# Optimization experiments

Measured on AMD Instinct MI355X. Metric: run time of the kernel, lower is better.

## Reference

```python
import jax, jax.numpy as jnp
import numpy as np
from jax import lax

H = 8  # hardcoded in the module (node indices 0..7)


def setup_inputs() -> dict:
    k = jax.random.key(0)
    k1, k2, k3, k4, k5 = jax.random.split(k, 5)
    B, S, D = 1024, 7, 4096  # seq MUST be 7 (Conv1d uses it as channels)
    query = jax.random.normal(k1, (B, S, D), jnp.float32)
    key = jax.random.normal(k2, (B, S, D), jnp.float32)
    value = jax.random.normal(k3, (B, S, D), jnp.float32)
    conv_w = jax.random.normal(k4, (7, 7, 3), jnp.float32) * 0.05  # Conv1d(7,7,3) OIW
    conv_b = jnp.zeros((7,), jnp.float32)
    w_out = jax.random.normal(k5, (D, D), jnp.float32) * 0.02  # linears[-1].weight
    b_out = jnp.zeros((D,), jnp.float32)
    return {"query": query, "key": key, "value": value,
            "conv_w": conv_w, "conv_b": conv_b, "w_out": w_out, "b_out": b_out}


def reference(query, key, value, conv_w, conv_b, w_out, b_out):
    B, S, D = query.shape
    dk = D // H
    # split q/k/v into H chunks of d_k along last dim -> [B, H, S, dk]
    split = lambda t: jnp.moveaxis(t.reshape(B, S, H, dk), 2, 1)
    q, kk, v = split(query), split(key), split(value)
    # node_i = cat(key_i, value_i, query_i) -> [B, H, S, 3dk]
    node = jnp.concatenate([kk, v, q], axis=-1)
    # neighbor sums along the head axis: s0=n0+n1, s_i=n_{i-1}+n_i+n_{i+1}, s7=n6+n7
    npad = jnp.pad(node, ((0, 0), (1, 1), (0, 0), (0, 0)))
    s = npad[:, :-2] + npad[:, 1:-1] + npad[:, 2:]  # [B, H, S, 3dk]
    # shared Conv1d(7,7,3,stride=1,pad=1) over the 3dk axis; channels = S = 7
    x = s.reshape(B * H, S, 3 * dk)
    x = lax.conv_general_dilated(x, conv_w, window_strides=(1,), padding=((1, 1),),
                                 dimension_numbers=("NCW", "OIW", "NCW"))
    x = x + conv_b[None, :, None]
    x = x.reshape(B, H, S, 3 * dk)
    # re-split: [0]=k', [1]=v', [2]=q'; attention(q', k', v')
    k2, v2, q2 = x[..., :dk], x[..., dk:2 * dk], x[..., 2 * dk:]
    scores = jnp.einsum("bhqd,bhkd->bhqk", q2, k2) * (1.0 / (dk ** 0.5))
    p = jax.nn.softmax(scores, axis=-1)
    atn = jnp.einsum("bhqk,bhkd->bhqd", p, v2)  # [B, H, S, dk]
    out = jnp.moveaxis(atn, 1, 2).reshape(B, S, D)  # concat heads
    return out @ w_out.T + b_out  # linears[-1]
```

## Files before the change

kernel.cpp:

```cpp
#include <hip/hip_runtime.h>
#include <hip/hip_bf16.h>

#define Hh 8
#define Bb 1024
#define Ss 7
#define Dd 4096
#define DK 512
#define Mrows (Bb*Ss)
#define RS 520

typedef float  f32x4  __attribute__((ext_vector_type(4)));
typedef float  f32x2  __attribute__((ext_vector_type(2)));
typedef short  bf16x8 __attribute__((ext_vector_type(8)));

static __device__ __forceinline__ unsigned short f2bf(float f) {
  union { float f; unsigned int u; } v; v.f = f;
  unsigned int u = v.u;
  u += 0x7FFFu + ((u >> 16) & 1u);
  return (unsigned short)(u >> 16);
}

static __device__ __forceinline__ void gload_lds16(const void* g, void* l) {
  __builtin_amdgcn_global_load_lds(
      (const __attribute__((address_space(1))) unsigned int*)g,
      (__attribute__((address_space(3))) unsigned int*)l,
      16, 0, 0);
}

static __device__ __forceinline__ float sum3s(const float* __restrict__ src, int b, int i, int h, int c) {
  long base = (long)(b * Ss + i) * Dd + h * DK + c;
  float v = src[base];
  if (h > 0) v += src[base - DK];
  if (h < 7) v += src[base + DK];
  return v;
}

__global__ __launch_bounds__(256, 5) void attn_kernel(
    const float* __restrict__ qg, const float* __restrict__ kg, const float* __restrict__ vg,
    const float* __restrict__ cw, const float* __restrict__ cb,
    unsigned short* __restrict__ Abf)
{
  __shared__ float bufA[Ss][RS];
  __shared__ float bufB[Ss][RS];
  __shared__ float cw4[49][4];
  __shared__ float cb_s[7];
  __shared__ float scores_s[49];
  __shared__ float pmat[7][7];

  const int t    = threadIdx.x;
  const int bh   = blockIdx.x;
  const int b    = bh >> 3, h = bh & 7;
  const int lane = t & 63, wave = t >> 6;

  if (t < 147) { int oi = t / 3; cw4[oi][t - oi * 3] = cw[t]; }
  if (t < 7) {
    cb_s[t] = cb[t];
    bufA[t][3]   = 0.f;
    bufA[t][516] = sum3s(vg, b, t, h, 0);
    bufB[t][3]   = sum3s(vg, b, t, h, 511);
    bufB[t][516] = 0.f;
  }

  #pragma unroll
  for (int j = 0; j < 7; ++j) {
    int slot = j * 256 + t;
    int isK  = slot < 896;
    int s2   = isK ? slot : slot - 896;
    int i    = s2 >> 7, c4 = (s2 & 127) << 2;
    const float* src = isK ? kg : qg;
    float* dst = isK ? &bufA[i][4 + c4] : &bufB[i][4 + c4];
    long base = (long)(b * Ss + i) * Dd + h * DK + c4;
    float4 v = *(const float4*)(src + base);
    if (h > 0) { float4 a = *(const float4*)(src + base - DK); v.x+=a.x; v.y+=a.y; v.z+=a.z; v.w+=a.w; }
    if (h < 7) { float4 a = *(const float4*)(src + base + DK); v.x+=a.x; v.y+=a.y; v.z+=a.z; v.w+=a.w; }
    *(float4*)dst = v;
  }
  __syncthreads();

  const int w2 = 2 * t;
  float ok0[7], ok1[7], oq0[7], oq1[7];
  #pragma unroll
  for (int o = 0; o < 7; ++o) { float c0 = cb_s[o]; ok0[o]=c0; ok1[o]=c0; oq0[o]=c0; oq1[o]=c0; }
  #pragma unroll
  for (int i = 0; i < 7; ++i) {
    float a0 = bufA[i][3+w2], a1 = bufA[i][4+w2], a2 = bufA[i][5+w2], a3 = bufA[i][6+w2];
    float q0 = bufB[i][3+w2], q1 = bufB[i][4+w2], q2 = bufB[i][5+w2], q3 = bufB[i][6+w2];
    #pragma unroll
    for (int o = 0; o < 7; ++o) {
      f32x4 wv = *(const f32x4*)&cw4[o*7+i][0];
      ok0[o] += wv[0]*a0 + wv[1]*a1 + wv[2]*a2;
      ok1[o] += wv[0]*a1 + wv[1]*a2 + wv[2]*a3;
      oq0[o] += wv[0]*q0 + wv[1]*q1 + wv[2]*q2;
      oq1[o] += wv[0]*q1 + wv[1]*q2 + wv[2]*q3;
    }
  }
  __syncthreads();
  #pragma unroll
  for (int o = 0; o < 7; ++o) {
    *(f32x2*)&bufA[o][4 + w2] = (f32x2){ok0[o], ok1[o]};
    *(f32x2*)&bufB[o][4 + w2] = (f32x2){oq0[o], oq1[o]};
  }
  __syncthreads();

  for (int p = wave; p < 49; p += 4) {
    int qq = p / 7, kk = p - qq * 7;
    f32x4 x0 = *(const f32x4*)&bufB[qq][4 + lane * 4];
    f32x4 x1 = *(const f32x4*)&bufB[qq][4 + 256 + lane * 4];
    f32x4 y0 = *(const f32x4*)&bufA[kk][4 + lane * 4];
    f32x4 y1 = *(const f32x4*)&bufA[kk][4 + 256 + lane * 4];
    float part = x0[0]*y0[0] + x0[1]*y0[1] + x0[2]*y0[2] + x0[3]*y0[3]
               + x1[0]*y1[0] + x1[1]*y1[1] + x1[2]*y1[2] + x1[3]*y1[3];
    #pragma unroll
    for (int off = 32; off; off >>= 1) part += __shfl_xor(part, off);
    if (lane == 0) scores_s[p] = part * 0.044194173824159216f;
  }
  __syncthreads();

  if (t < 7) {
    float row[7], m = -1e30f;
    #pragma unroll
    for (int k = 0; k < 7; ++k) { row[k] = scores_s[t * 7 + k]; m = fmaxf(m, row[k]); }
    float s = 0.f;
    #pragma unroll
    for (int k = 0; k < 7; ++k) { row[k] = __expf(row[k] - m); s += row[k]; }
    float inv = 1.0f / s;
    #pragma unroll
    for (int k = 0; k < 7; ++k) pmat[t][k] = row[k] * inv;
    bufB[t][3]   = sum3s(kg, b, t, h, 511);
    bufB[t][516] = sum3s(qg, b, t, h, 0);
  }
  #pragma unroll
  for (int j = 0; j < 4; ++j) {
    int slot = j * 256 + t;
    if (slot < 896) {
      int i = slot >> 7, c4 = (slot & 127) << 2;
      long base = (long)(b * Ss + i) * Dd + h * DK + c4;
      float4 v = *(const float4*)(vg + base);
      if (h > 0) { float4 a = *(const float4*)(vg + base - DK); v.x+=a.x; v.y+=a.y; v.z+=a.z; v.w+=a.w; }
      if (h < 7) { float4 a = *(const float4*)(vg + base + DK); v.x+=a.x; v.y+=a.y; v.z+=a.z; v.w+=a.w; }
      *(float4*)&bufB[i][4 + c4] = v;
    }
  }
  __syncthreads();

  float ov0[7], ov1[7];
  #pragma unroll
  for (int o = 0; o < 7; ++o) { float c0 = cb_s[o]; ov0[o] = c0; ov1[o] = c0; }
  #pragma unroll
  for (int i = 0; i < 7; ++i) {
    float v0 = bufB[i][3+w2], v1 = bufB[i][4+w2], v2 = bufB[i][5+w2], v3 = bufB[i][6+w2];
    #pragma unroll
    for (int o = 0; o < 7; ++o) {
      f32x4 wv = *(const f32x4*)&cw4[o*7+i][0];
      ov0[o] += wv[0]*v0 + wv[1]*v1 + wv[2]*v2;
      ov1[o] += wv[0]*v1 + wv[1]*v2 + wv[2]*v3;
    }
  }
  #pragma unroll
  for (int qq = 0; qq < 7; ++qq) {
    float a0 = 0.f, a1 = 0.f;
    #pragma unroll
    for (int k = 0; k < 7; ++k) { float pk = pmat[qq][k]; a0 += pk * ov0[k]; a1 += pk * ov1[k]; }
    unsigned int packed = ((unsigned int)f2bf(a1) << 16) | (unsigned int)f2bf(a0);
    *(unsigned int*)&Abf[(long)(b * Ss + qq) * Dd + h * DK + w2] = packed;
  }
}

__global__ __launch_bounds__(256) void castw(const float* __restrict__ w, unsigned short* __restrict__ o)
{
  const int total = (Dd * Dd) / 4;
  for (int s = blockIdx.x * 256 + threadIdx.x; s < total; s += gridDim.x * 256) {
    float4 f = *(const float4*)(w + (long)s * 4);
    ushort4 u;
    u.x = f2bf(f.x); u.y = f2bf(f.y); u.z = f2bf(f.z); u.w = f2bf(f.w);
    *(ushort4*)(o + (long)s * 4) = u;
  }
}

#define BM 128
#define BN 128
#define BK 32
#define NTILES (Dd / BN)
#define MTILES (Mrows / BM)

__global__ __launch_bounds__(256) void gemm_bt(
    const unsigned short* __restrict__ A, const unsigned short* __restrict__ Bt,
    const float* __restrict__ bias, float* __restrict__ C)
{
  __shared__ unsigned short As[BM * BK];
  __shared__ unsigned short Bs[BN * BK];

  const int wg = blockIdx.x;
  const int sw = (wg & 7) * (NTILES * MTILES / 8) + (wg >> 3);
  const int m0 = (sw >> 5) * BM;
  const int n0 = (sw & 31) * BN;

  const int t    = threadIdx.x;
  const int wave = t >> 6, lane = t & 63;
  const int wm   = (wave >> 1) * 64, wn = (wave & 1) * 64;
  const int lr   = lane & 15, lk = (lane >> 4) * 8;

  const int srow = t >> 2;
  const int scol = (t & 3) * 8;

  f32x4 acc[4][4] = {};

  for (int kt = 0; kt < Dd / BK; ++kt) {
    const int k0 = kt * BK;
    #pragma unroll
    for (int j = 0; j < 2; ++j) {
      const int row = j * 64 + srow;
      gload_lds16(A  + (long)(m0 + row) * Dd + k0 + scol, &As[row * BK + scol]);
      gload_lds16(Bt + (long)(n0 + row) * Dd + k0 + scol, &Bs[row * BK + scol]);
    }
    __syncthreads();

    bf16x8 af[4], bfr[4];
    #pragma unroll
    for (int mi = 0; mi < 4; ++mi) af[mi]  = *(const bf16x8*)&As[(wm + mi * 16 + lr) * BK + lk];
    #pragma unroll
    for (int ni = 0; ni < 4; ++ni) bfr[ni] = *(const bf16x8*)&Bs[(wn + ni * 16 + lr) * BK + lk];
    #pragma unroll
    for (int mi = 0; mi < 4; ++mi)
      #pragma unroll
      for (int ni = 0; ni < 4; ++ni)
        acc[mi][ni] = __builtin_amdgcn_mfma_f32_16x16x32_bf16(af[mi], bfr[ni], acc[mi][ni], 0, 0, 0);
    __syncthreads();
  }

  #pragma unroll
  for (int ni = 0; ni < 4; ++ni) {
    const int col = n0 + wn + ni * 16 + lr;
    const float bi = bias[col];
    #pragma unroll
    for (int mi = 0; mi < 4; ++mi) {
      const int rbase = m0 + wm + mi * 16 + (lane >> 4) * 4;
      #pragma unroll
      for (int r = 0; r < 4; ++r)
        C[(long)(rbase + r) * Dd + col] = acc[mi][ni][r] + bi;
    }
  }
}

extern "C" void kernel_launch(void* const* d_in, const int* in_sizes, int n_in,
                              void* d_out, int out_size, void* d_ws, size_t ws_size,
                              hipStream_t stream) {
  const float* qg = (const float*)d_in[0];
  const float* kg = (const float*)d_in[1];
  const float* vg = (const float*)d_in[2];
  const float* cw = (const float*)d_in[3];
  const float* cb = (const float*)d_in[4];
  const float* wo = (const float*)d_in[5];
  const float* bo = (const float*)d_in[6];
  float* out = (float*)d_out;

  unsigned short* Abf = (unsigned short*)d_ws;
  unsigned short* Wbf = Abf + (size_t)Mrows * Dd;

  hipLaunchKernelGGL(castw,       dim3(2048),    dim3(256), 0, stream, wo, Wbf);
  hipLaunchKernelGGL(attn_kernel, dim3(Bb * Hh), dim3(256), 0, stream, qg, kg, vg, cw, cb, Abf);
  hipLaunchKernelGGL(gemm_bt,     dim3(NTILES * MTILES), dim3(256), 0, stream, Abf, Wbf, bo, out);
}
```

Baseline: 1.019 ms.

## Split K/Q conv into sequential passes, remap attn blocks, drop GEMM swizzle

The attention kernel now computes the K and Q convolutions in two sequential passes that reuse one pair of accumulator arrays, which cuts register pressure. Its occupancy hint of 5 blocks per CU is removed. Attention blocks are remapped with an XCD-style interleave so that neighbouring (b,h) blocks land on the same die. The GEMM drops its XCD tile swizzle in favour of a plain 2D grid, which may hurt L2 reuse across chiplets, and the extra barrier between the two conv passes adds some synchronisation.

```diff
diff --git a/kernel.cpp b/kernel.cpp
--- a/kernel.cpp
+++ b/kernel.cpp
@@ -35,7 +35,7 @@
   return v;
 }
 
-__global__ __launch_bounds__(256, 5) void attn_kernel(
+__global__ __launch_bounds__(256) void attn_kernel(
     const float* __restrict__ qg, const float* __restrict__ kg, const float* __restrict__ vg,
     const float* __restrict__ cw, const float* __restrict__ cb,
     unsigned short* __restrict__ Abf)
@@ -48,7 +48,8 @@
   __shared__ float pmat[7][7];
 
   const int t    = threadIdx.x;
-  const int bh   = blockIdx.x;
+  const int g    = blockIdx.x;
+  const int bh   = (g & 7) * (Bb * Hh / 8) + (g >> 3);
   const int b    = bh >> 3, h = bh & 7;
   const int lane = t & 63, wave = t >> 6;
 
@@ -78,28 +79,41 @@
   __syncthreads();
 
   const int w2 = 2 * t;
-  float ok0[7], ok1[7], oq0[7], oq1[7];
-  #pragma unroll
-  for (int o = 0; o < 7; ++o) { float c0 = cb_s[o]; ok0[o]=c0; ok1[o]=c0; oq0[o]=c0; oq1[o]=c0; }
+
+  float c0a[7], c1a[7];
+  #pragma unroll
+  for (int o = 0; o < 7; ++o) { c0a[o] = cb_s[o]; c1a[o] = cb_s[o]; }
   #pragma unroll
   for (int i = 0; i < 7; ++i) {
     float a0 = bufA[i][3+w2], a1 = bufA[i][4+w2], a2 = bufA[i][5+w2], a3 = bufA[i][6+w2];
-    float q0 = bufB[i][3+w2], q1 = bufB[i][4+w2], q2 = bufB[i][5+w2], q3 = bufB[i][6+w2];
     #pragma unroll
     for (int o = 0; o < 7; ++o) {
       f32x4 wv = *(const f32x4*)&cw4[o*7+i][0];
-      ok0[o] += wv[0]*a0 + wv[1]*a1 + wv[2]*a2;
-      ok1[o] += wv[0]*a1 + wv[1]*a2 + wv[2]*a3;
-      oq0[o] += wv[0]*q0 + wv[1]*q1 + wv[2]*q2;
-      oq1[o] += wv[0]*q1 + wv[1]*q2 + wv[2]*q3;
-    }
-  }
-  __syncthreads();
-  #pragma unroll
-  for (int o = 0; o < 7; ++o) {
-    *(f32x2*)&bufA[o][4 + w2] = (f32x2){ok0[o], ok1[o]};
-    *(f32x2*)&bufB[o][4 + w2] = (f32x2){oq0[o], oq1[o]};
-  }
+      c0a[o] += wv[0]*a0 + wv[1]*a1 + wv[2]*a2;
+      c1a[o] += wv[0]*a1 + wv[1]*a2 + wv[2]*a3;
+    }
+  }
+  __syncthreads();
+  #pragma unroll
+  for (int o = 0; o < 7; ++o)
+    *(f32x2*)&bufA[o][4 + w2] = (f32x2){c0a[o], c1a[o]};
+
+  #pragma unroll
+  for (int o = 0; o < 7; ++o) { c0a[o] = cb_s[o]; c1a[o] = cb_s[o]; }
+  #pragma unroll
+  for (int i = 0; i < 7; ++i) {
+    float a0 = bufB[i][3+w2], a1 = bufB[i][4+w2], a2 = bufB[i][5+w2], a3 = bufB[i][6+w2];
+    #pragma unroll
+    for (int o = 0; o < 7; ++o) {
+      f32x4 wv = *(const f32x4*)&cw4[o*7+i][0];
+      c0a[o] += wv[0]*a0 + wv[1]*a1 + wv[2]*a2;
+      c1a[o] += wv[0]*a1 + wv[1]*a2 + wv[2]*a3;
+    }
+  }
+  __syncthreads();
+  #pragma unroll
+  for (int o = 0; o < 7; ++o)
+    *(f32x2*)&bufB[o][4 + w2] = (f32x2){c0a[o], c1a[o]};
   __syncthreads();
 
   for (int p = wave; p < 49; p += 4) {
@@ -145,7 +159,7 @@
 
   float ov0[7], ov1[7];
   #pragma unroll
-  for (int o = 0; o < 7; ++o) { float c0 = cb_s[o]; ov0[o] = c0; ov1[o] = c0; }
+  for (int o = 0; o < 7; ++o) { ov0[o] = cb_s[o]; ov1[o] = cb_s[o]; }
   #pragma unroll
   for (int i = 0; i < 7; ++i) {
     float v0 = bufB[i][3+w2], v1 = bufB[i][4+w2], v2 = bufB[i][5+w2], v3 = bufB[i][6+w2];
@@ -180,8 +194,6 @@
 #define BM 128
 #define BN 128
 #define BK 32
-#define NTILES (Dd / BN)
-#define MTILES (Mrows / BM)
 
 __global__ __launch_bounds__(256) void gemm_bt(
     const unsigned short* __restrict__ A, const unsigned short* __restrict__ Bt,
@@ -190,12 +202,9 @@
   __shared__ unsigned short As[BM * BK];
   __shared__ unsigned short Bs[BN * BK];
 
-  const int wg = blockIdx.x;
-  const int sw = (wg & 7) * (NTILES * MTILES / 8) + (wg >> 3);
-  const int m0 = (sw >> 5) * BM;
-  const int n0 = (sw & 31) * BN;
-
   const int t    = threadIdx.x;
+  const int m0   = blockIdx.y * BM;
+  const int n0   = blockIdx.x * BN;
   const int wave = t >> 6, lane = t & 63;
   const int wm   = (wave >> 1) * 64, wn = (wave & 1) * 64;
   const int lr   = lane & 15, lk = (lane >> 4) * 8;
@@ -259,5 +268,5 @@
 
   hipLaunchKernelGGL(castw,       dim3(2048),    dim3(256), 0, stream, wo, Wbf);
   hipLaunchKernelGGL(attn_kernel, dim3(Bb * Hh), dim3(256), 0, stream, qg, kg, vg, cw, cb, Abf);
-  hipLaunchKernelGGL(gemm_bt,     dim3(NTILES * MTILES), dim3(256), 0, stream, Abf, Wbf, bo, out);
-}
+  hipLaunchKernelGGL(gemm_bt,     dim3(Dd / BN, Mrows / BM), dim3(256), 0, stream, Abf, Wbf, bo, out);
+}
```

Result: faster. 822.5 us (-19.2%).
